# Optimization experiments

Measured on AMD Instinct MI355X. Metric: run time of the kernel, lower is better.

## Reference

```python
import jax, jax.numpy as jnp
import numpy as np

B, S, D = 4, 2048, 1024
M, CH = 16, 256  # experts, chunk size (4096 // 16)


def make_preds(m):
    # Watts-Strogatz ring lattice (n=m, k=4), edges oriented min->max => DAG.
    preds = []
    for v in range(m):
        p = set()
        if v >= 1:
            p.add(v - 1)
        if v >= 2:
            p.add(v - 2)
        if v == m - 2:
            p.add(0)          # wrap edge {m-2, 0}
        if v == m - 1:
            p.update((0, 1))  # wrap edges {m-1, 0}, {m-1, 1}
        preds.append(sorted(p))
    return preds

PREDS = make_preds(M)


def layernorm(x, g, b, eps=1e-5):
    mu = x.mean(-1, keepdims=True)
    var = ((x - mu) ** 2).mean(-1, keepdims=True)
    return (x - mu) * jax.lax.rsqrt(var + eps) * g + b


def setup_inputs() -> dict:
    key = jax.random.key(0)
    ks = jax.random.split(key, 8)
    sc_in = 1.0 / np.sqrt(D)
    sc_ch = 1.0 / np.sqrt(CH)
    return {
        "x": jax.random.normal(ks[0], (B, S, D), jnp.float32),
        "norm_g": jnp.ones((D,), jnp.float32),
        "norm_b": jnp.zeros((D,), jnp.float32),
        "fc1_w": jax.random.normal(ks[1], (M, CH, D), jnp.float32) * sc_in,
        "fc1_b": jax.random.normal(ks[2], (M, CH), jnp.float32) * 0.02,
        "ln_g": jnp.ones((M, CH), jnp.float32),
        "ln_b": jnp.zeros((M, CH), jnp.float32),
        "fc2_w": jax.random.normal(ks[3], (M, D, CH), jnp.float32) * sc_ch,
        "fc2_bias": jax.random.normal(ks[4], (D,), jnp.float32) * 0.02,
        "router_w": jax.random.normal(ks[5], (M, 4, D), jnp.float32) * sc_in,
        "router_b": jax.random.normal(ks[6], (M, 4), jnp.float32) * 0.02,
    }


def reference(x, norm_g, norm_b, fc1_w, fc1_b, ln_g, ln_b, fc2_w, fc2_bias,
              router_w, router_b):
    m = fc1_w.shape[0]
    x_norm = layernorm(x, norm_g, norm_b)
    outs = []
    for v in range(m):  # 0..m-1 is a topological order (all edges low->high)
        pv = PREDS[v]
        if pv:
            npred = len(pv)
            logits = jnp.einsum('bsd,pd->bsp', x_norm, router_w[v, :npred]) \
                     + router_b[v, :npred]
            w = jax.nn.sigmoid(logits)                                # [B,S,P]
            pred_stack = jnp.stack([outs[u] for u in pv], axis=-1)    # [B,S,D,P]
            node_in = jnp.einsum('bsdp,bsp->bsd', pred_stack, w)
        else:
            node_in = x_norm
        h = jax.nn.gelu(jnp.einsum('bsd,cd->bsc', node_in, fc1_w[v]) + fc1_b[v],
                        approximate=False)
        h = layernorm(h, ln_g[v], ln_b[v])
        outs.append(jnp.einsum('bsc,dc->bsd', h, fc2_w[v]))  # fc2 bias zeroed per-node
    combined = outs[m - 1] + fc2_bias  # node m-1 is the unique terminal node
    return x + combined  # use_residual=True
```

## Files before the change

kernel.cpp:

```cpp
#include <hip/hip_runtime.h>
#include <hip/hip_bf16.h>

typedef _Float16 f16;
typedef _Float16 f16x8 __attribute__((ext_vector_type(8)));
typedef float f32x4 __attribute__((ext_vector_type(4)));

#define TOKS 8192
#define DDIM 1024
#define CHDIM 256

__device__ __constant__ int c_OFF[16]  = {0,0,1,3,5,7,9,11,13,15,17,19,21,23,25,28};
__device__ __constant__ int c_NP[16]   = {0,1,2,2,2,2,2,2,2,2,2,2,2,2,3,4};
__device__ __constant__ int c_RROW[32] = {4, 8,9, 12,13, 16,17, 20,21, 24,25, 28,29, 32,33, 36,37, 40,41, 44,45, 48,49, 52,53, 56,57,58, 60,61,62,63};

__device__ __forceinline__ f16x8 sp8(f16 w){
  f16x8 r;
  #pragma unroll
  for (int j=0;j<8;++j) r[j]=w;
  return r;
}

__global__ __launch_bounds__(256) void k_prep(const float* __restrict__ x, const float* __restrict__ g,
                                              const float* __restrict__ b, f16* __restrict__ xn,
                                              const float* __restrict__ rw, const float* __restrict__ rb,
                                              float* __restrict__ wsig,
                                              const float* __restrict__ w1, const float* __restrict__ w2,
                                              f16* __restrict__ w1p, f16* __restrict__ w2p){
  const int blk = blockIdx.x, tid = threadIdx.x;
  if (blk < 2048){
    const int lane = tid & 63, wv = tid >> 6;
    const int tk = blk*4 + wv;
    const float* xp = x + (size_t)tk*DDIM + lane*16;
    float xv[16];
    #pragma unroll
    for (int j=0;j<16;j+=4){ const float4 f=*(const float4*)(xp+j); xv[j]=f.x; xv[j+1]=f.y; xv[j+2]=f.z; xv[j+3]=f.w; }
    float s=0.f, q=0.f;
    #pragma unroll
    for (int j=0;j<16;++j){ s += xv[j]; q += xv[j]*xv[j]; }
    #pragma unroll
    for (int m=1;m<64;m<<=1){ s += __shfl_xor(s,m); q += __shfl_xor(q,m); }
    const float mu = s*(1.f/DDIM);
    const float rs = rsqrtf(q*(1.f/DDIM) - mu*mu + 1e-5f);
    #pragma unroll
    for (int j=0;j<16;j+=4){
      const float4 gg=*(const float4*)(g + lane*16 + j);
      const float4 bb=*(const float4*)(b + lane*16 + j);
      xv[j]   = (xv[j]  -mu)*rs*gg.x + bb.x;
      xv[j+1] = (xv[j+1]-mu)*rs*gg.y + bb.y;
      xv[j+2] = (xv[j+2]-mu)*rs*gg.z + bb.z;
      xv[j+3] = (xv[j+3]-mu)*rs*gg.w + bb.w;
    }
    f16x8 o0, o1;
    #pragma unroll
    for (int j=0;j<8;++j){ o0[j] = (f16)xv[j]; o1[j] = (f16)xv[8+j]; }
    *(f16x8*)(xn + (size_t)tk*DDIM + lane*16)     = o0;
    *(f16x8*)(xn + (size_t)tk*DDIM + lane*16 + 8) = o1;
    for (int e=0;e<32;++e){
      const int row = c_RROW[e];
      const float* rp = rw + (size_t)row*DDIM + lane*16;
      float d = 0.f;
      #pragma unroll
      for (int j=0;j<16;j+=4){
        const float4 f=*(const float4*)(rp+j);
        d += xv[j]*f.x + xv[j+1]*f.y + xv[j+2]*f.z + xv[j+3]*f.w;
      }
      #pragma unroll
      for (int m=1;m<64;m<<=1) d += __shfl_xor(d,m);
      if (lane==0) wsig[tk*32 + e] = 1.f/(1.f + expf(-(d + rb[row])));
    }
  } else if (blk < 4096){
    const int c = (blk-2048)*256 + tid;
    const int l15 = c & 15, g4 = (c>>4)&3, ic = (c>>6)&31, wvv = (c>>11)&15, v = c>>15;
    const float* s = w1 + (size_t)v*262144 + (size_t)(wvv*16 + l15)*1024 + ic*32 + g4*8;
    const float4 a = *(const float4*)s, b4 = *(const float4*)(s+4);
    f16x8 o;
    o[0]=(f16)a.x; o[1]=(f16)a.y; o[2]=(f16)a.z; o[3]=(f16)a.w;
    o[4]=(f16)b4.x; o[5]=(f16)b4.y; o[6]=(f16)b4.z; o[7]=(f16)b4.w;
    *(f16x8*)(w1p + (size_t)c*8) = o;
  } else {
    const int c = (blk-4096)*256 + tid;
    const int l15 = c & 15, g4 = (c>>4)&3, nf = (c>>6)&3, ks = (c>>8)&7, wvv = (c>>11)&15, v = c>>15;
    const float* s = w2 + (size_t)v*262144 + (size_t)(wvv*64 + nf*16 + l15)*256 + ks*32 + g4*8;
    const float4 a = *(const float4*)s, b4 = *(const float4*)(s+4);
    f16x8 o;
    o[0]=(f16)a.x; o[1]=(f16)a.y; o[2]=(f16)a.z; o[3]=(f16)a.w;
    o[4]=(f16)b4.x; o[5]=(f16)b4.y; o[6]=(f16)b4.z; o[7]=(f16)b4.w;
    *(f16x8*)(w2p + (size_t)c*8) = o;
  }
}

__global__ __launch_bounds__(1024,4) void k_moe(
    const f16* __restrict__ xn, const f16* __restrict__ w1p, const f16* __restrict__ w2p,
    const float* __restrict__ fc1b, const float* __restrict__ lng, const float* __restrict__ lnb,
    const float* __restrict__ f2bias, const float* __restrict__ wsigG,
    const float* __restrict__ x, float* __restrict__ out, f16* __restrict__ gouts)
{
  __shared__ f16 wsg[32][32];
  __shared__ __align__(16) f16 Pbuf0[32*1032];
  __shared__ __align__(16) f16 Pbuf1[32*1032];
  __shared__ __align__(16) f16 hln[32*264];
  __shared__ float part[32][17][2];
  __shared__ float musq[32][2];

  const int tid = threadIdx.x;
  const int lane = tid & 63, wv = tid >> 6;
  const int l15 = lane & 15, g4 = (lane >> 4) & 3;
  const int blk = blockIdx.x, tok0 = blk * 32;
  const f32x4 fzero = {0.f,0.f,0.f,0.f};

  wsg[tid>>5][tid&31] = (f16)wsigG[tok0*32 + tid];

  f16* Pp = Pbuf0;
  f16* Pc = Pbuf1;

  for (int v=0; v<16; ++v){
    const f16* bp1 = w1p + (size_t)(v*16 + wv)*16384 + lane*8;
    f16x8 pb[12];
    #pragma unroll
    for (int j=0;j<12;++j) pb[j] = *(const f16x8*)(bp1 + j*512);

    if (v == 0){
      #pragma unroll
      for (int p=0;p<4;++p){
        const int c = tid + p*1024, t = c>>7, c8 = (c&127)*8;
        *(f16x8*)&Pc[t*1032 + c8] = *(const f16x8*)(xn + (size_t)(tok0+t)*DDIM + c8);
      }
    } else {
      const int np = c_NP[v], off = c_OFF[v];
      const int ech = off + np - 1, ev2 = off + np - 2, nex = np - 2;
      #pragma unroll
      for (int p=0;p<4;++p){
        const int c = tid + p*1024, t = c>>7, c8 = (c&127)*8;
        const f16x8 pv = *(const f16x8*)&Pp[t*1032 + c8];
        if (v <= 2)
          *(f16x8*)(gouts + (size_t)(v-1)*TOKS*DDIM + (size_t)(tok0+t)*DDIM + c8) = pv;
        f16x8 acc = sp8(wsg[t][ech]) * pv;
        if (np >= 2){
          const f16x8 p2 = *(const f16x8*)&Pc[t*1032 + c8];
          acc += sp8(wsg[t][ev2]) * p2;
        }
        if (nex >= 1){
          const f16x8 e0 = *(const f16x8*)(gouts + (size_t)(tok0+t)*DDIM + c8);
          acc += sp8(wsg[t][off]) * e0;
        }
        if (nex >= 2){
          const f16x8 e1 = *(const f16x8*)(gouts + (size_t)TOKS*DDIM + (size_t)(tok0+t)*DDIM + c8);
          acc += sp8(wsg[t][off+1]) * e1;
        }
        *(f16x8*)&Pc[t*1032 + c8] = acc;
      }
    }
    __syncthreads();

    f32x4 acc1[2] = {fzero, fzero};
    #pragma unroll
    for (int ic=0; ic<32; ++ic){
      const f16x8 b = pb[ic%12];
      if (ic < 20) pb[ic%12] = *(const f16x8*)(bp1 + (ic+12)*512);
      const f16x8 a0 = *(const f16x8*)&Pc[l15*1032      + ic*32 + g4*8];
      const f16x8 a1 = *(const f16x8*)&Pc[(16+l15)*1032 + ic*32 + g4*8];
      acc1[0] = __builtin_amdgcn_mfma_f32_16x16x32_f16(a0, b, acc1[0], 0,0,0);
      acc1[1] = __builtin_amdgcn_mfma_f32_16x16x32_f16(a1, b, acc1[1], 0,0,0);
    }

    const f16* bp2 = w2p + (size_t)(v*16 + wv)*16384 + lane*8;
    f16x8 pc2[12];
    #pragma unroll
    for (int j=0;j<12;++j) pc2[j] = *(const f16x8*)(bp2 + j*512);

    const int c1 = wv*16 + l15;
    const float fb = fc1b[v*CHDIM + c1];
    const float lg = lng[v*CHDIM + c1], lb = lnb[v*CHDIM + c1];
    #pragma unroll
    for (int mf=0;mf<2;++mf)
      #pragma unroll
      for (int r=0;r<4;++r){
        const float h = acc1[mf][r] + fb;
        acc1[mf][r] = 0.5f*h*(1.f + erff(h*0.70710678118654752f));
      }
    #pragma unroll
    for (int mf=0;mf<2;++mf)
      #pragma unroll
      for (int r=0;r<4;++r){
        float s = acc1[mf][r], q = s*s;
        #pragma unroll
        for (int m=1;m<16;m<<=1){ s += __shfl_xor(s,m); q += __shfl_xor(q,m); }
        if (l15==0){ const int t = mf*16 + g4*4 + r; part[t][wv][0]=s; part[t][wv][1]=q; }
      }
    __syncthreads();
    if (tid < 32){
      float s=0.f, q=0.f;
      #pragma unroll
      for (int w=0;w<16;++w){ s += part[tid][w][0]; q += part[tid][w][1]; }
      const float mu = s*(1.f/CHDIM);
      musq[tid][0] = mu;
      musq[tid][1] = rsqrtf(q*(1.f/CHDIM) - mu*mu + 1e-5f);
    }
    __syncthreads();
    #pragma unroll
    for (int mf=0;mf<2;++mf)
      #pragma unroll
      for (int r=0;r<4;++r){
        const int t = mf*16 + g4*4 + r;
        hln[t*264 + c1] = (f16)((acc1[mf][r]-musq[t][0])*musq[t][1]*lg + lb);
      }
    __syncthreads();

    f32x4 acc2[2][4];
    #pragma unroll
    for (int mf=0;mf<2;++mf)
      #pragma unroll
      for (int nf=0;nf<4;++nf) acc2[mf][nf] = fzero;
    f16x8 a0h, a1h;
    #pragma unroll
    for (int cki=0; cki<32; ++cki){
      const int ks = cki>>2, nf = cki&3;
      if (nf == 0){
        a0h = *(const f16x8*)&hln[l15*264      + ks*32 + g4*8];
        a1h = *(const f16x8*)&hln[(16+l15)*264 + ks*32 + g4*8];
      }
      const f16x8 b = pc2[cki%12];
      if (cki < 20) pc2[cki%12] = *(const f16x8*)(bp2 + (cki+12)*512);
      acc2[0][nf] = __builtin_amdgcn_mfma_f32_16x16x32_f16(a0h, b, acc2[0][nf], 0,0,0);
      acc2[1][nf] = __builtin_amdgcn_mfma_f32_16x16x32_f16(a1h, b, acc2[1][nf], 0,0,0);
    }
    #pragma unroll
    for (int mf=0;mf<2;++mf)
      #pragma unroll
      for (int nf=0;nf<4;++nf){
        const int c2 = wv*64 + nf*16 + l15;
        const float fb2 = (v==15) ? f2bias[c2] : 0.f;
        #pragma unroll
        for (int r=0;r<4;++r){
          const int t = mf*16 + g4*4 + r;
          Pc[t*1032 + c2] = (f16)(acc2[mf][nf][r] + fb2);
        }
      }
    __syncthreads();

    if (v == 15){
      #pragma unroll
      for (int p=0;p<4;++p){
        const int c = tid + p*1024, t = c>>7, c8 = (c&127)*8;
        const f16x8 val = *(const f16x8*)&Pc[t*1032 + c8];
        const size_t gi = (size_t)(tok0+t)*DDIM + c8;
        const float4 x0 = *(const float4*)(x+gi), x1 = *(const float4*)(x+gi+4);
        float4 o0, o1;
        o0.x = x0.x + (float)val[0]; o0.y = x0.y + (float)val[1];
        o0.z = x0.z + (float)val[2]; o0.w = x0.w + (float)val[3];
        o1.x = x1.x + (float)val[4]; o1.y = x1.y + (float)val[5];
        o1.z = x1.z + (float)val[6]; o1.w = x1.w + (float)val[7];
        *(float4*)(out+gi) = o0; *(float4*)(out+gi+4) = o1;
      }
    }
    f16* tmp = Pp; Pp = Pc; Pc = tmp;
  }
}

extern "C" void kernel_launch(void* const* d_in, const int* in_sizes, int n_in,
                              void* d_out, int out_size, void* d_ws, size_t ws_size,
                              hipStream_t stream) {
  (void)in_sizes; (void)n_in; (void)out_size; (void)ws_size;
  const float* x   = (const float*)d_in[0];
  const float* ng  = (const float*)d_in[1];
  const float* nb_ = (const float*)d_in[2];
  const float* w1  = (const float*)d_in[3];
  const float* f1b = (const float*)d_in[4];
  const float* lg  = (const float*)d_in[5];
  const float* lb  = (const float*)d_in[6];
  const float* w2  = (const float*)d_in[7];
  const float* f2b = (const float*)d_in[8];
  const float* rw  = (const float*)d_in[9];
  const float* rb  = (const float*)d_in[10];
  float* out = (float*)d_out;

  char* ws = (char*)d_ws;
  f16*  xnh  = (f16*)(ws);
  f16*  w1p  = (f16*)(ws + 16777216);
  f16*  w2p  = (f16*)(ws + 16777216 + 8388608);
  float* wsg = (float*)(ws + 16777216 + 8388608 + 8388608);
  f16*  gouts= (f16*)(ws + 16777216 + 8388608 + 8388608 + 1048576);

  k_prep<<<6144, 256, 0, stream>>>(x, ng, nb_, xnh, rw, rb, wsg, w1, w2, w1p, w2p);
  k_moe<<<256, 1024, 0, stream>>>(xnh, w1p, w2p, f1b, lg, lb, f2b, wsg, x, out, gouts);
}
```

Measured before the change: 394.8 us.

## Fuse next-node input mixing into fc2 epilogue and prefetch next fc1 weights

Computes the next node's weighted predecessor mix directly in the fc2 epilogue (writing both the raw output and the mixed input). This removes the separate mixing pass and its barrier for most nodes; only nodes 14-15 still need an extra pass for the wrap-edge inputs. It also shrinks the weight prefetch register buffers from 12 to 8 and loads the first fc1 weights of the next node during the tail of the fc2 loop. The pointer swap at the end of the loop and the amdgpu attributes replace launch_bounds. The risk is subtle buffer aliasing between the two buffers, plus added epilogue work on the critical path.

```diff
diff --git a/kernel.cpp b/kernel.cpp
--- a/kernel.cpp
+++ b/kernel.cpp
@@ -89,7 +89,8 @@
   }
 }
 
-__global__ __launch_bounds__(1024,4) void k_moe(
+__global__ __attribute__((amdgpu_flat_work_group_size(1024,1024), amdgpu_waves_per_eu(4,4)))
+void k_moe(
     const f16* __restrict__ xn, const f16* __restrict__ w1p, const f16* __restrict__ w2p,
     const float* __restrict__ fc1b, const float* __restrict__ lng, const float* __restrict__ lnb,
     const float* __restrict__ f2bias, const float* __restrict__ wsigG,
@@ -113,50 +114,53 @@
   f16* Pp = Pbuf0;
   f16* Pc = Pbuf1;
 
+  #pragma unroll
+  for (int p=0;p<4;++p){
+    const int c = tid + p*1024, t = c>>7, c8 = (c&127)*8;
+    *(f16x8*)&Pc[t*1032 + c8] = *(const f16x8*)(xn + (size_t)(tok0+t)*DDIM + c8);
+  }
+  f16x8 pb[8];
+  {
+    const f16* b0 = w1p + (size_t)(0*16 + wv)*16384 + lane*8;
+    #pragma unroll
+    for (int j=0;j<8;++j) pb[j] = *(const f16x8*)(b0 + j*512);
+  }
+  __syncthreads();
+
+  #pragma unroll 1
   for (int v=0; v<16; ++v){
     const f16* bp1 = w1p + (size_t)(v*16 + wv)*16384 + lane*8;
-    f16x8 pb[12];
-    #pragma unroll
-    for (int j=0;j<12;++j) pb[j] = *(const f16x8*)(bp1 + j*512);
-
-    if (v == 0){
+
+    if (v == 1 || v == 2){
       #pragma unroll
       for (int p=0;p<4;++p){
         const int c = tid + p*1024, t = c>>7, c8 = (c&127)*8;
-        *(f16x8*)&Pc[t*1032 + c8] = *(const f16x8*)(xn + (size_t)(tok0+t)*DDIM + c8);
-      }
-    } else {
-      const int np = c_NP[v], off = c_OFF[v];
-      const int ech = off + np - 1, ev2 = off + np - 2, nex = np - 2;
+        *(f16x8*)(gouts + (size_t)(v-1)*TOKS*DDIM + (size_t)(tok0+t)*DDIM + c8)
+          = *(const f16x8*)&Pp[t*1032 + c8];
+      }
+    }
+    if (v >= 14){
+      const int off = c_OFF[v];
       #pragma unroll
       for (int p=0;p<4;++p){
         const int c = tid + p*1024, t = c>>7, c8 = (c&127)*8;
-        const f16x8 pv = *(const f16x8*)&Pp[t*1032 + c8];
-        if (v <= 2)
-          *(f16x8*)(gouts + (size_t)(v-1)*TOKS*DDIM + (size_t)(tok0+t)*DDIM + c8) = pv;
-        f16x8 acc = sp8(wsg[t][ech]) * pv;
-        if (np >= 2){
-          const f16x8 p2 = *(const f16x8*)&Pc[t*1032 + c8];
-          acc += sp8(wsg[t][ev2]) * p2;
+        f16x8 a = *(const f16x8*)&Pc[t*1032 + c8];
+        const f16x8 e0 = *(const f16x8*)(gouts + (size_t)(tok0+t)*DDIM + c8);
+        a += sp8(wsg[t][off]) * e0;
+        if (v == 15){
+          const f16x8 e1 = *(const f16x8*)(gouts + (size_t)TOKS*DDIM + (size_t)(tok0+t)*DDIM + c8);
+          a += sp8(wsg[t][off+1]) * e1;
         }
-        if (nex >= 1){
-          const f16x8 e0 = *(const f16x8*)(gouts + (size_t)(tok0+t)*DDIM + c8);
-          acc += sp8(wsg[t][off]) * e0;
-        }
-        if (nex >= 2){
-          const f16x8 e1 = *(const f16x8*)(gouts + (size_t)TOKS*DDIM + (size_t)(tok0+t)*DDIM + c8);
-          acc += sp8(wsg[t][off+1]) * e1;
-        }
-        *(f16x8*)&Pc[t*1032 + c8] = acc;
-      }
-    }
-    __syncthreads();
+        *(f16x8*)&Pc[t*1032 + c8] = a;
+      }
+      __syncthreads();
+    }
 
     f32x4 acc1[2] = {fzero, fzero};
     #pragma unroll
     for (int ic=0; ic<32; ++ic){
-      const f16x8 b = pb[ic%12];
-      if (ic < 20) pb[ic%12] = *(const f16x8*)(bp1 + (ic+12)*512);
+      const f16x8 b = pb[ic&7];
+      if (ic < 24) pb[ic&7] = *(const f16x8*)(bp1 + (ic+8)*512);
       const f16x8 a0 = *(const f16x8*)&Pc[l15*1032      + ic*32 + g4*8];
       const f16x8 a1 = *(const f16x8*)&Pc[(16+l15)*1032 + ic*32 + g4*8];
       acc1[0] = __builtin_amdgcn_mfma_f32_16x16x32_f16(a0, b, acc1[0], 0,0,0);
@@ -164,9 +168,9 @@
     }
 
     const f16* bp2 = w2p + (size_t)(v*16 + wv)*16384 + lane*8;
-    f16x8 pc2[12];
-    #pragma unroll
-    for (int j=0;j<12;++j) pc2[j] = *(const f16x8*)(bp2 + j*512);
+    f16x8 pc2[8];
+    #pragma unroll
+    for (int j=0;j<8;++j) pc2[j] = *(const f16x8*)(bp2 + j*512);
 
     const int c1 = wv*16 + l15;
     const float fb = fc1b[v*CHDIM + c1];
@@ -206,6 +210,7 @@
       }
     __syncthreads();
 
+    const f16* bp1n = w1p + (size_t)((v+1)*16 + wv)*16384 + lane*8;
     f32x4 acc2[2][4];
     #pragma unroll
     for (int mf=0;mf<2;++mf)
@@ -219,23 +224,45 @@
         a0h = *(const f16x8*)&hln[l15*264      + ks*32 + g4*8];
         a1h = *(const f16x8*)&hln[(16+l15)*264 + ks*32 + g4*8];
       }
-      const f16x8 b = pc2[cki%12];
-      if (cki < 20) pc2[cki%12] = *(const f16x8*)(bp2 + (cki+12)*512);
+      const f16x8 b = pc2[cki&7];
+      if (cki < 24) pc2[cki&7] = *(const f16x8*)(bp2 + (cki+8)*512);
+      else if (v < 15) pb[cki-24] = *(const f16x8*)(bp1n + (cki-24)*512);
       acc2[0][nf] = __builtin_amdgcn_mfma_f32_16x16x32_f16(a0h, b, acc2[0][nf], 0,0,0);
       acc2[1][nf] = __builtin_amdgcn_mfma_f32_16x16x32_f16(a1h, b, acc2[1][nf], 0,0,0);
     }
-    #pragma unroll
-    for (int mf=0;mf<2;++mf)
-      #pragma unroll
-      for (int nf=0;nf<4;++nf){
-        const int c2 = wv*64 + nf*16 + l15;
-        const float fb2 = (v==15) ? f2bias[c2] : 0.f;
+
+    if (v < 15){
+      const int w = v+1, npw = c_NP[w], offw = c_OFF[w];
+      const int ech = offw + npw - 1, ev2 = offw + npw - 2;
+      #pragma unroll
+      for (int mf=0;mf<2;++mf)
         #pragma unroll
-        for (int r=0;r<4;++r){
-          const int t = mf*16 + g4*4 + r;
-          Pc[t*1032 + c2] = (f16)(acc2[mf][nf][r] + fb2);
+        for (int nf=0;nf<4;++nf){
+          const int c2 = wv*64 + nf*16 + l15;
+          #pragma unroll
+          for (int r=0;r<4;++r){
+            const int t = mf*16 + g4*4 + r;
+            const float o = acc2[mf][nf][r];
+            float ain = (float)wsg[t][ech] * o;
+            if (npw >= 2) ain += (float)wsg[t][ev2] * (float)Pp[t*1032 + c2];
+            Pc[t*1032 + c2] = (f16)o;
+            Pp[t*1032 + c2] = (f16)ain;
+          }
         }
-      }
+    } else {
+      #pragma unroll
+      for (int mf=0;mf<2;++mf)
+        #pragma unroll
+        for (int nf=0;nf<4;++nf){
+          const int c2 = wv*64 + nf*16 + l15;
+          const float fb2 = f2bias[c2];
+          #pragma unroll
+          for (int r=0;r<4;++r){
+            const int t = mf*16 + g4*4 + r;
+            Pc[t*1032 + c2] = (f16)(acc2[mf][nf][r] + fb2);
+          }
+        }
+    }
     __syncthreads();
 
     if (v == 15){
```

After: 606.9 us. +53.8%, slower.

## Fold hidden LayerNorm normalization into fc2 epilogue to drop two barriers

Applied to the files above, without the earlier changes.

Rewrites LN(h)·W2ᵀ as rs·(h·g)·W2ᵀ − rs·mu·(W2·g) + W2·b, with W2·g and W2·b precomputed per expert in the prep kernel. The fc2 MMA now consumes unnormalized h scaled by gamma, and the per-token mean and rstd come from the stored partial sums, reduced by shuffles in the epilogue. This removes two __syncthreads and a serial 32-thread reduction per expert. In exchange it does extra shuffle work, adds fp16 rounding of unnormalized activations before fc2, and adds 64 prep blocks.

```diff
diff --git a/kernel.cpp b/kernel.cpp
--- a/kernel.cpp
+++ b/kernel.cpp
@@ -25,7 +25,9 @@
                                               const float* __restrict__ rw, const float* __restrict__ rb,
                                               float* __restrict__ wsig,
                                               const float* __restrict__ w1, const float* __restrict__ w2,
-                                              f16* __restrict__ w1p, f16* __restrict__ w2p){
+                                              f16* __restrict__ w1p, f16* __restrict__ w2p,
+                                              const float* __restrict__ lng, const float* __restrict__ lnb,
+                                              float* __restrict__ w2g, float* __restrict__ w2lb){
   const int blk = blockIdx.x, tid = threadIdx.x;
   if (blk < 2048){
     const int lane = tid & 63, wv = tid >> 6;
@@ -77,7 +79,7 @@
     o[0]=(f16)a.x; o[1]=(f16)a.y; o[2]=(f16)a.z; o[3]=(f16)a.w;
     o[4]=(f16)b4.x; o[5]=(f16)b4.y; o[6]=(f16)b4.z; o[7]=(f16)b4.w;
     *(f16x8*)(w1p + (size_t)c*8) = o;
-  } else {
+  } else if (blk < 6144){
     const int c = (blk-4096)*256 + tid;
     const int l15 = c & 15, g4 = (c>>4)&3, nf = (c>>6)&3, ks = (c>>8)&7, wvv = (c>>11)&15, v = c>>15;
     const float* s = w2 + (size_t)v*262144 + (size_t)(wvv*64 + nf*16 + l15)*256 + ks*32 + g4*8;
@@ -86,12 +88,30 @@
     o[0]=(f16)a.x; o[1]=(f16)a.y; o[2]=(f16)a.z; o[3]=(f16)a.w;
     o[4]=(f16)b4.x; o[5]=(f16)b4.y; o[6]=(f16)b4.z; o[7]=(f16)b4.w;
     *(f16x8*)(w2p + (size_t)c*8) = o;
+  } else {
+    const int idx = (blk-6144)*256 + tid;
+    const int v = idx >> 10, d = idx & 1023;
+    const float* wr = w2 + (size_t)v*262144 + (size_t)d*256;
+    const float* gr = lng + v*256;
+    const float* br = lnb + v*256;
+    float sg=0.f, sb=0.f;
+    #pragma unroll 4
+    for (int c=0;c<256;c+=4){
+      const float4 w4  = *(const float4*)(wr+c);
+      const float4 g4v = *(const float4*)(gr+c);
+      const float4 b4v = *(const float4*)(br+c);
+      sg += w4.x*g4v.x + w4.y*g4v.y + w4.z*g4v.z + w4.w*g4v.w;
+      sb += w4.x*b4v.x + w4.y*b4v.y + w4.z*b4v.z + w4.w*b4v.w;
+    }
+    w2g[v*DDIM + d]  = sg;
+    w2lb[v*DDIM + d] = sb;
   }
 }
 
 __global__ __launch_bounds__(1024,4) void k_moe(
     const f16* __restrict__ xn, const f16* __restrict__ w1p, const f16* __restrict__ w2p,
-    const float* __restrict__ fc1b, const float* __restrict__ lng, const float* __restrict__ lnb,
+    const float* __restrict__ fc1b, const float* __restrict__ lng,
+    const float* __restrict__ w2g, const float* __restrict__ w2lb,
     const float* __restrict__ f2bias, const float* __restrict__ wsigG,
     const float* __restrict__ x, float* __restrict__ out, f16* __restrict__ gouts)
 {
@@ -100,7 +120,6 @@
   __shared__ __align__(16) f16 Pbuf1[32*1032];
   __shared__ __align__(16) f16 hln[32*264];
   __shared__ float part[32][17][2];
-  __shared__ float musq[32][2];
 
   const int tid = threadIdx.x;
   const int lane = tid & 63, wv = tid >> 6;
@@ -170,7 +189,7 @@
 
     const int c1 = wv*16 + l15;
     const float fb = fc1b[v*CHDIM + c1];
-    const float lg = lng[v*CHDIM + c1], lb = lnb[v*CHDIM + c1];
+    const float lg = lng[v*CHDIM + c1];
     #pragma unroll
     for (int mf=0;mf<2;++mf)
       #pragma unroll
@@ -187,22 +206,12 @@
         for (int m=1;m<16;m<<=1){ s += __shfl_xor(s,m); q += __shfl_xor(q,m); }
         if (l15==0){ const int t = mf*16 + g4*4 + r; part[t][wv][0]=s; part[t][wv][1]=q; }
       }
-    __syncthreads();
-    if (tid < 32){
-      float s=0.f, q=0.f;
-      #pragma unroll
-      for (int w=0;w<16;++w){ s += part[tid][w][0]; q += part[tid][w][1]; }
-      const float mu = s*(1.f/CHDIM);
-      musq[tid][0] = mu;
-      musq[tid][1] = rsqrtf(q*(1.f/CHDIM) - mu*mu + 1e-5f);
-    }
-    __syncthreads();
     #pragma unroll
     for (int mf=0;mf<2;++mf)
       #pragma unroll
       for (int r=0;r<4;++r){
         const int t = mf*16 + g4*4 + r;
-        hln[t*264 + c1] = (f16)((acc1[mf][r]-musq[t][0])*musq[t][1]*lg + lb);
+        hln[t*264 + c1] = (f16)(acc1[mf][r]*lg);
       }
     __syncthreads();
 
@@ -224,8 +233,28 @@
       acc2[0][nf] = __builtin_amdgcn_mfma_f32_16x16x32_f16(a0h, b, acc2[0][nf], 0,0,0);
       acc2[1][nf] = __builtin_amdgcn_mfma_f32_16x16x32_f16(a1h, b, acc2[1][nf], 0,0,0);
     }
-    #pragma unroll
-    for (int mf=0;mf<2;++mf)
+
+    float wgv[4], wbv[4];
+    #pragma unroll
+    for (int nf=0;nf<4;++nf){
+      const int c2 = wv*64 + nf*16 + l15;
+      wgv[nf] = w2g[v*DDIM + c2];
+      wbv[nf] = w2lb[v*DDIM + c2];
+    }
+    #pragma unroll
+    for (int mf=0;mf<2;++mf){
+      float rs4[4], rm4[4];
+      #pragma unroll
+      for (int r=0;r<4;++r){
+        const int t = mf*16 + g4*4 + r;
+        const float2 pq = *(const float2*)&part[t][l15][0];
+        float s = pq.x, q = pq.y;
+        #pragma unroll
+        for (int m=1;m<16;m<<=1){ s += __shfl_xor(s,m); q += __shfl_xor(q,m); }
+        const float mu = s*(1.f/CHDIM);
+        rs4[r] = rsqrtf(q*(1.f/CHDIM) - mu*mu + 1e-5f);
+        rm4[r] = rs4[r]*mu;
+      }
       #pragma unroll
       for (int nf=0;nf<4;++nf){
         const int c2 = wv*64 + nf*16 + l15;
@@ -233,9 +262,10 @@
         #pragma unroll
         for (int r=0;r<4;++r){
           const int t = mf*16 + g4*4 + r;
-          Pc[t*1032 + c2] = (f16)(acc2[mf][nf][r] + fb2);
+          Pc[t*1032 + c2] = (f16)(rs4[r]*acc2[mf][nf][r] - rm4[r]*wgv[nf] + wbv[nf] + fb2);
         }
       }
+    }
     __syncthreads();
 
     if (v == 15){
@@ -278,9 +308,12 @@
   f16*  xnh  = (f16*)(ws);
   f16*  w1p  = (f16*)(ws + 16777216);
   f16*  w2p  = (f16*)(ws + 16777216 + 8388608);
-  float* wsg = (float*)(ws + 16777216 + 8388608 + 8388608);
-  f16*  gouts= (f16*)(ws + 16777216 + 8388608 + 8388608 + 1048576);
-
-  k_prep<<<6144, 256, 0, stream>>>(x, ng, nb_, xnh, rw, rb, wsg, w1, w2, w1p, w2p);
-  k_moe<<<256, 1024, 0, stream>>>(xnh, w1p, w2p, f1b, lg, lb, f2b, wsg, x, out, gouts);
+  float* wsg = (float*)(ws + 33554432);
+  float* w2g = (float*)(ws + 33554432 + 1048576);
+  float* w2lb= (float*)(ws + 33554432 + 1048576 + 65536);
+  f16*  gouts= (f16*)(ws + 33554432 + 1048576 + 131072);
+
+  k_prep<<<6208, 256, 0, stream>>>(x, ng, nb_, xnh, rw, rb, wsg, w1, w2, w1p, w2p,
+                                   lg, lb, w2g, w2lb);
+  k_moe<<<256, 1024, 0, stream>>>(xnh, w1p, w2p, f1b, lg, w2g, w2lb, f2b, wsg, x, out, gouts);
 }
```

Result: slower. 449.8 us (+13.9%).

## Split fc1 GEMM across K halves per wave and shuffle-reduce layernorm stats

Applied to the files above, without the earlier changes.

The fc1 GEMM work is split so each wave computes 32 output channels over half of K, instead of 16 channels over the full K. Each A fragment read from LDS now feeds two MFMAs, which halves A-operand shared-memory traffic. The weight pre-pack is reordered to match. The two K-half partial sums are combined through LDS in fp16, which adds rounding error, and only half the waves run GELU and layernorm. The serial single-thread layernorm statistic reduction is replaced by a per-wave shuffle reduction over the partials, removing the musq stage.

```diff
diff --git a/kernel.cpp b/kernel.cpp
--- a/kernel.cpp
+++ b/kernel.cpp
@@ -70,8 +70,9 @@
     }
   } else if (blk < 4096){
     const int c = (blk-2048)*256 + tid;
-    const int l15 = c & 15, g4 = (c>>4)&3, ic = (c>>6)&31, wvv = (c>>11)&15, v = c>>15;
-    const float* s = w1 + (size_t)v*262144 + (size_t)(wvv*16 + l15)*1024 + ic*32 + g4*8;
+    const int l15 = c & 15, g4 = (c>>4)&3, nf = (c>>6)&1, ic = (c>>7)&15, wvv = (c>>11)&15, v = c>>15;
+    const int ng = wvv & 7, kh = wvv >> 3;
+    const float* s = w1 + (size_t)v*262144 + (size_t)(ng*32 + nf*16 + l15)*1024 + kh*512 + ic*32 + g4*8;
     const float4 a = *(const float4*)s, b4 = *(const float4*)(s+4);
     f16x8 o;
     o[0]=(f16)a.x; o[1]=(f16)a.y; o[2]=(f16)a.z; o[3]=(f16)a.w;
@@ -99,12 +100,12 @@
   __shared__ __align__(16) f16 Pbuf0[32*1032];
   __shared__ __align__(16) f16 Pbuf1[32*1032];
   __shared__ __align__(16) f16 hln[32*264];
-  __shared__ float part[32][17][2];
-  __shared__ float musq[32][2];
+  __shared__ float part[32][9][2];
 
   const int tid = threadIdx.x;
   const int lane = tid & 63, wv = tid >> 6;
   const int l15 = lane & 15, g4 = (lane >> 4) & 3;
+  const int ng = wv & 7, kh = wv >> 3;
   const int blk = blockIdx.x, tok0 = blk * 32;
   const f32x4 fzero = {0.f,0.f,0.f,0.f};
 
@@ -152,15 +153,21 @@
     }
     __syncthreads();
 
-    f32x4 acc1[2] = {fzero, fzero};
-    #pragma unroll
-    for (int ic=0; ic<32; ++ic){
-      const f16x8 b = pb[ic%12];
-      if (ic < 20) pb[ic%12] = *(const f16x8*)(bp1 + (ic+12)*512);
-      const f16x8 a0 = *(const f16x8*)&Pc[l15*1032      + ic*32 + g4*8];
-      const f16x8 a1 = *(const f16x8*)&Pc[(16+l15)*1032 + ic*32 + g4*8];
-      acc1[0] = __builtin_amdgcn_mfma_f32_16x16x32_f16(a0, b, acc1[0], 0,0,0);
-      acc1[1] = __builtin_amdgcn_mfma_f32_16x16x32_f16(a1, b, acc1[1], 0,0,0);
+    f32x4 acc1[2][2];
+    acc1[0][0]=fzero; acc1[0][1]=fzero; acc1[1][0]=fzero; acc1[1][1]=fzero;
+    const int kbase = kh*512;
+    f16x8 a0, a1;
+    #pragma unroll
+    for (int j=0;j<32;++j){
+      const int ic = j>>1, nf = j&1;
+      const f16x8 b = pb[j%12];
+      if (j < 20) pb[j%12] = *(const f16x8*)(bp1 + (j+12)*512);
+      if (nf == 0){
+        a0 = *(const f16x8*)&Pc[l15*1032      + kbase + ic*32 + g4*8];
+        a1 = *(const f16x8*)&Pc[(16+l15)*1032 + kbase + ic*32 + g4*8];
+      }
+      acc1[0][nf] = __builtin_amdgcn_mfma_f32_16x16x32_f16(a0, b, acc1[0][nf], 0,0,0);
+      acc1[1][nf] = __builtin_amdgcn_mfma_f32_16x16x32_f16(a1, b, acc1[1][nf], 0,0,0);
     }
 
     const f16* bp2 = w2p + (size_t)(v*16 + wv)*16384 + lane*8;
@@ -168,42 +175,74 @@
     #pragma unroll
     for (int j=0;j<12;++j) pc2[j] = *(const f16x8*)(bp2 + j*512);
 
-    const int c1 = wv*16 + l15;
-    const float fb = fc1b[v*CHDIM + c1];
-    const float lg = lng[v*CHDIM + c1], lb = lnb[v*CHDIM + c1];
-    #pragma unroll
-    for (int mf=0;mf<2;++mf)
-      #pragma unroll
-      for (int r=0;r<4;++r){
-        const float h = acc1[mf][r] + fb;
-        acc1[mf][r] = 0.5f*h*(1.f + erff(h*0.70710678118654752f));
-      }
-    #pragma unroll
-    for (int mf=0;mf<2;++mf)
-      #pragma unroll
-      for (int r=0;r<4;++r){
-        float s = acc1[mf][r], q = s*s;
-        #pragma unroll
-        for (int m=1;m<16;m<<=1){ s += __shfl_xor(s,m); q += __shfl_xor(q,m); }
-        if (l15==0){ const int t = mf*16 + g4*4 + r; part[t][wv][0]=s; part[t][wv][1]=q; }
-      }
-    __syncthreads();
-    if (tid < 32){
-      float s=0.f, q=0.f;
-      #pragma unroll
-      for (int w=0;w<16;++w){ s += part[tid][w][0]; q += part[tid][w][1]; }
-      const float mu = s*(1.f/CHDIM);
-      musq[tid][0] = mu;
-      musq[tid][1] = rsqrtf(q*(1.f/CHDIM) - mu*mu + 1e-5f);
-    }
-    __syncthreads();
-    #pragma unroll
-    for (int mf=0;mf<2;++mf)
-      #pragma unroll
-      for (int r=0;r<4;++r){
-        const int t = mf*16 + g4*4 + r;
-        hln[t*264 + c1] = (f16)((acc1[mf][r]-musq[t][0])*musq[t][1]*lg + lb);
-      }
+    if (kh == 1){
+      #pragma unroll
+      for (int mf=0;mf<2;++mf)
+        #pragma unroll
+        for (int nf=0;nf<2;++nf){
+          const int c = ng*32 + nf*16 + l15;
+          #pragma unroll
+          for (int r=0;r<4;++r){
+            const int t = mf*16 + g4*4 + r;
+            hln[t*264 + c] = (f16)acc1[mf][nf][r];
+          }
+        }
+    }
+    __syncthreads();
+
+    float lgv[2], lbv[2];
+    #pragma unroll
+    for (int nf=0;nf<2;++nf){
+      const int c = ng*32 + nf*16 + l15;
+      lgv[nf] = lng[v*CHDIM + c];
+      lbv[nf] = lnb[v*CHDIM + c];
+    }
+    if (kh == 0){
+      #pragma unroll
+      for (int nf=0;nf<2;++nf){
+        const int c = ng*32 + nf*16 + l15;
+        const float fbv = fc1b[v*CHDIM + c];
+        #pragma unroll
+        for (int mf=0;mf<2;++mf)
+          #pragma unroll
+          for (int r=0;r<4;++r){
+            const int t = mf*16 + g4*4 + r;
+            const float h = acc1[mf][nf][r] + (float)hln[t*264 + c] + fbv;
+            acc1[mf][nf][r] = 0.5f*h*(1.f + erff(h*0.70710678118654752f));
+          }
+      }
+      #pragma unroll
+      for (int mf=0;mf<2;++mf)
+        #pragma unroll
+        for (int r=0;r<4;++r){
+          float s = acc1[mf][0][r] + acc1[mf][1][r];
+          float q = acc1[mf][0][r]*acc1[mf][0][r] + acc1[mf][1][r]*acc1[mf][1][r];
+          #pragma unroll
+          for (int m=1;m<16;m<<=1){ s += __shfl_xor(s,m); q += __shfl_xor(q,m); }
+          if (l15==0){ const int t = mf*16 + g4*4 + r; part[t][ng][0]=s; part[t][ng][1]=q; }
+        }
+    }
+    __syncthreads();
+
+    if (kh == 0){
+      #pragma unroll
+      for (int mf=0;mf<2;++mf)
+        #pragma unroll
+        for (int r=0;r<4;++r){
+          const int t = mf*16 + g4*4 + r;
+          const float2 pq = *(const float2*)&part[t][l15&7][0];
+          float s = pq.x, q = pq.y;
+          #pragma unroll
+          for (int m=1;m<16;m<<=1){ s += __shfl_xor(s,m); q += __shfl_xor(q,m); }
+          const float mu = s*(1.f/(2.f*CHDIM));
+          const float rs = rsqrtf(q*(1.f/(2.f*CHDIM)) - mu*mu + 1e-5f);
+          #pragma unroll
+          for (int nf=0;nf<2;++nf){
+            const int c = ng*32 + nf*16 + l15;
+            hln[t*264 + c] = (f16)((acc1[mf][nf][r]-mu)*rs*lgv[nf] + lbv[nf]);
+          }
+        }
+    }
     __syncthreads();
 
     f32x4 acc2[2][4];
@@ -278,8 +317,8 @@
   f16*  xnh  = (f16*)(ws);
   f16*  w1p  = (f16*)(ws + 16777216);
   f16*  w2p  = (f16*)(ws + 16777216 + 8388608);
-  float* wsg = (float*)(ws + 16777216 + 8388608 + 8388608);
-  f16*  gouts= (f16*)(ws + 16777216 + 8388608 + 8388608 + 1048576);
+  float* wsg = (float*)(ws + 33554432);
+  f16*  gouts= (f16*)(ws + 33554432 + 1048576);
 
   k_prep<<<6144, 256, 0, stream>>>(x, ng, nb_, xnh, rw, rb, wsg, w1, w2, w1p, w2p);
   k_moe<<<256, 1024, 0, stream>>>(xnh, w1p, w2p, f1b, lg, lb, f2b, wsg, x, out, gouts);
```

New measurement: 456.7 us. 1.16x slower.
